# Kernel tuning notes

Measured on AMD Instinct MI355X. Metric: run time of the kernel, lower is better.

Reference implementation:

```python
import jax, jax.numpy as jnp
import numpy as np
import math

N_BLOCKS, DEPTH, K = 5, 10, 2


def build_dilations():
    # Mirrors WaveNet.__init__: list of (new_dilation, init_dilation) per layer.
    dil = []
    init = 1
    for _ in range(N_BLOCKS):
        new = 1
        for _ in range(DEPTH):
            dil.append((new, init))
            init = new
            new *= 2
    return dil


def conv1d_k2(x, w):
    # x: [N, Cin, L], w: [Cout, Cin, 2]; VALID conv -> [N, Cout, L-1]
    return jax.lax.conv_general_dilated(x, w, (1,), 'VALID',
                                        dimension_numbers=('NCH', 'OIH', 'NCH'))


def pw(x, w):
    # 1x1 conv: x [N, Cin, L], w [Cout, Cin]
    return jnp.einsum('oi,nil->nol', w, x)


def dilate(x, dilation, init_dilation):
    # Faithful port of the pytorch-wavenet dilate(): refolds time into batch.
    # All shape arithmetic is static Python ints (jit-safe).
    r = dilation / init_dilation
    if r == 1:
        return x
    n, c, l = x.shape
    new_l = int(math.ceil(l / r) * r)
    if new_l != l:
        x = jnp.pad(x, ((0, 0), (0, 0), (new_l - l, 0)))  # pad_start with zeros
        l = new_l
    l_new = int(round(l * init_dilation / dilation))
    n_new = int(round(n * dilation / init_dilation))
    x = jnp.transpose(x, (1, 2, 0)).reshape(c, l_new, n_new)  # (c, l, n) row-major view
    return jnp.transpose(x, (2, 0, 1))


def wavenet_forward(tokens, emb, pre_w, filt_w, gate_w, res_w, skip_w,
                    post_w1, post_b1, post_w2, post_b2):
    # preprocess: embedding -> [B, C_res, L], then causal k=2 conv (length preserved)
    x = jnp.transpose(emb[tokens], (0, 2, 1))
    x = conv1d_k2(jnp.pad(x, ((0, 0), (0, 0), (K - 1, 0))), pre_w)
    skip = None
    for i, (d, init_d) in enumerate(build_dilations()):
        xd = dilate(x, d, init_d)                       # fold/unfold to dilation d
        z = jnp.tanh(conv1d_k2(xd, filt_w[i])) * jax.nn.sigmoid(conv1d_k2(xd, gate_w[i]))
        s = pw(dilate(z, 1, d), skip_w[i])              # skip contribution, unfolded
        x = pw(z, res_w[i]) + xd[:, :, K - 1:]          # residual connection (folded)
        skip = s if skip is None else skip[:, :, -s.shape[2]:] + s
    h = jax.nn.relu(skip)
    h = jax.nn.relu(pw(h, post_w1) + post_b1[None, :, None])
    return pw(h, post_w2) + post_b2[None, :, None]


def setup_inputs() -> dict:
    key = jax.random.key(0)
    ks = jax.random.split(key, 11)
    B, L = 4, 8192
    V, Cr, Cd, Cs, Ce = 256, 32, 32, 512, 256
    NL = N_BLOCKS * DEPTH
    f = lambda k, shape: jax.random.normal(k, shape, jnp.float32) * 0.1
    return {
        'tokens': jax.random.randint(ks[0], (B, L), 0, V, dtype=jnp.int32),
        'emb': f(ks[1], (V, Cr)),
        'pre_w': f(ks[2], (Cr, Cr, K)),
        'filt_w': f(ks[3], (NL, Cd, Cr, K)),
        'gate_w': f(ks[4], (NL, Cd, Cr, K)),
        'res_w': f(ks[5], (NL, Cr, Cd)),
        'skip_w': f(ks[6], (NL, Cs, Cd)),
        'post_w1': f(ks[7], (Ce, Cs)),
        'post_b1': f(ks[8], (Ce,)),
        'post_w2': f(ks[9], (V, Ce)),
        'post_b2': f(ks[10], (V,)),
    }


def reference(tokens, emb, pre_w, filt_w, gate_w, res_w, skip_w,
              post_w1, post_b1, post_w2, post_b2):
    return wavenet_forward(tokens, emb, pre_w, filt_w, gate_w, res_w, skip_w,
                           post_w1, post_b1, post_w2, post_b2)
```

## Files before the change

### kernel.cpp

```cpp
#include <hip/hip_runtime.h>
#include <math.h>

#define NB 4
#define L0 8192
#define CR 32
#define CD 32
#define CS 512
#define CE 256
#define NV 256
#define OUT_T 5632
#define XSTRIDE 8192
#define NL 50
#define KCAT 1600

typedef __attribute__((ext_vector_type(8))) short  short8;
typedef __attribute__((ext_vector_type(4))) float  f32x4;
typedef __attribute__((ext_vector_type(4))) float  f4;
typedef __attribute__((ext_vector_type(4))) unsigned short us4;

static __device__ __forceinline__ unsigned short f2bf(float f) {
    unsigned int u = __builtin_bit_cast(unsigned int, f);
    u = (u + 0x7FFFu + ((u >> 16) & 1u)) >> 16;
    return (unsigned short)u;
}

__global__ __launch_bounds__(256) void k_prep(const float* __restrict__ sw,
                                              const float* __restrict__ w1,
                                              const float* __restrict__ w2,
                                              unsigned short* __restrict__ wsb,
                                              unsigned short* __restrict__ w1b,
                                              unsigned short* __restrict__ w2b)
{
    int idx = blockIdx.x * 256 + threadIdx.x;
    if (idx < NL * CS * CD) {
        int l = idx >> 14;
        int co = (idx >> 5) & 511;
        int c = idx & 31;
        wsb[co * KCAT + l * 32 + c] = f2bf(sw[idx]);
    } else if (idx < NL * CS * CD + CE * CS) {
        int e = idx - NL * CS * CD;
        w1b[e] = f2bf(w1[e]);
    } else {
        int e = idx - NL * CS * CD - CE * CS;
        w2b[e] = f2bf(w2[e]);
    }
}

__global__ __launch_bounds__(256) void k_pre(const int* __restrict__ tokens,
                                             const float* __restrict__ emb,
                                             const float* __restrict__ pw,
                                             float* __restrict__ x)
{
    int idx = blockIdx.x * 256 + threadIdx.x;
    int t = idx & (L0 - 1);
    int o = (idx >> 13) & 31;
    int b = idx >> 18;
    const int* tb = tokens + b * L0;
    int tok = tb[t];
    const float* e1 = emb + tok * CR;
    const float* w = pw + o * CR * 2;
    float acc = 0.f;
    if (t > 0) {
        const float* e0 = emb + tb[t - 1] * CR;
#pragma unroll
        for (int i = 0; i < CR; ++i)
            acc += w[i * 2] * e0[i] + w[i * 2 + 1] * e1[i];
    } else {
#pragma unroll
        for (int i = 0; i < CR; ++i)
            acc += w[i * 2 + 1] * e1[i];
    }
    x[(b * CR + o) * XSTRIDE + t] = acc;
}

__global__ __launch_bounds__(256) void k_layer(
    const float* __restrict__ x_in, float* __restrict__ x_out,
    unsigned short* __restrict__ Zt,
    const float* __restrict__ fw, const float* __restrict__ gw,
    const float* __restrict__ rw,
    int T_out, int d, int P, int skipOff, int kOff)
{
    __shared__ float As[32][68];
    __shared__ float Bs[32][68];
    __shared__ float Zs[32][68];
    __shared__ unsigned short ZsT[64][32];
    __shared__ float wfT[64][33];
    __shared__ float wgT[64][33];
    __shared__ float rwT[32][33];
    const int tid = threadIdx.x;
    const int t0 = blockIdx.x * 64;
    const int b = blockIdx.y;
    const float* xb = x_in + b * CR * XSTRIDE;

    for (int e = tid; e < 2048; e += 256) {
        int c = e >> 6, i2 = e & 63;
        wfT[i2][c] = fw[e];
        wgT[i2][c] = gw[e];
    }
    for (int e = tid; e < 1024; e += 256) {
        int c = e >> 5, i = e & 31;
        rwT[i][c] = rw[e];
    }
    {
        int ch = tid >> 3;
        int j0 = (tid & 7) * 8;
        const float* row = xb + ch * XSTRIDE;
#pragma unroll
        for (int k = 0; k < 8; ++k) {
            int t = t0 + j0 + k;
            float a = 0.f, bb = 0.f;
            if (t < T_out) {
                if (t >= P) a = row[t - P];
                bb = row[t + d - P];
            }
            As[ch][j0 + k] = a;
            Bs[ch][j0 + k] = bb;
        }
    }
    __syncthreads();
    {
        int c = tid & 31;
        int j0 = (tid >> 5) * 8;
        float af[8] = {0, 0, 0, 0, 0, 0, 0, 0};
        float ag[8] = {0, 0, 0, 0, 0, 0, 0, 0};
#pragma unroll
        for (int i = 0; i < 32; ++i) {
            float av[8], bv[8];
            *(f4*)&av[0] = *(const f4*)&As[i][j0];
            *(f4*)&av[4] = *(const f4*)&As[i][j0 + 4];
            *(f4*)&bv[0] = *(const f4*)&Bs[i][j0];
            *(f4*)&bv[4] = *(const f4*)&Bs[i][j0 + 4];
            float f0 = wfT[2 * i][c], f1 = wfT[2 * i + 1][c];
            float g0 = wgT[2 * i][c], g1 = wgT[2 * i + 1][c];
#pragma unroll
            for (int k = 0; k < 8; ++k) {
                af[k] += f0 * av[k] + f1 * bv[k];
                ag[k] += g0 * av[k] + g1 * bv[k];
            }
        }
#pragma unroll
        for (int k = 0; k < 8; ++k) {
            float e2a = __expf(2.f * af[k]);
            float th = 1.f - __fdividef(2.f, e2a + 1.f);
            float sg = __fdividef(1.f, 1.f + __expf(-ag[k]));
            float z = th * sg;
            Zs[c][j0 + k] = z;
            ZsT[j0 + k][c] = f2bf(z);
        }
    }
    __syncthreads();
    {
        int ch = tid >> 3;
        int j0 = (tid & 7) * 8;
        float accv[8];
        *(f4*)&accv[0] = *(const f4*)&Bs[ch][j0];
        *(f4*)&accv[4] = *(const f4*)&Bs[ch][j0 + 4];
#pragma unroll
        for (int i = 0; i < 32; ++i) {
            float w = rwT[i][ch];
            float zv[8];
            *(f4*)&zv[0] = *(const f4*)&Zs[i][j0];
            *(f4*)&zv[4] = *(const f4*)&Zs[i][j0 + 4];
#pragma unroll
            for (int k = 0; k < 8; ++k)
                accv[k] += w * zv[k];
        }
        float* orow = x_out + (b * CR + ch) * XSTRIDE;
#pragma unroll
        for (int k = 0; k < 8; ++k) {
            int t = t0 + j0 + k;
            if (t < T_out) orow[t] = accv[k];
        }
    }
    {
        int tl = tid >> 2;
        int cq = (tid & 3) * 8;
        int t = t0 + tl;
        if (t >= skipOff && t < T_out) {
            unsigned short* dst =
                Zt + ((size_t)b * OUT_T + (t - skipOff)) * KCAT + kOff + cq;
            *(short8*)dst = *(const short8*)&ZsT[tl][cq];
        }
    }
}

template <int MODE>
__global__ __launch_bounds__(256) void k_gemm(
    const unsigned short* __restrict__ A,
    const unsigned short* __restrict__ B,
    const float* __restrict__ bias,
    void* __restrict__ Cout, int M, int K)
{
    __shared__ unsigned short Asm[128][72];
    __shared__ unsigned short Bsm[64][72];
    const int tid = threadIdx.x;
    const int n0 = blockIdx.x * 64;
    const int m0 = blockIdx.y * 128;
    const int b = blockIdx.z;
    const unsigned short* Bb = B + (size_t)b * OUT_T * K;
    const int lane = tid & 63;
    const int wm = tid >> 6;
    f32x4 acc[2][4];
#pragma unroll
    for (int fm = 0; fm < 2; ++fm)
#pragma unroll
        for (int fn = 0; fn < 4; ++fn)
            acc[fm][fn] = (f32x4){0.f, 0.f, 0.f, 0.f};

    for (int kb = 0; kb < K; kb += 64) {
        __syncthreads();
#pragma unroll
        for (int it = 0; it < 4; ++it) {
            int lin = tid + it * 256;
            int row = lin >> 3, c8 = (lin & 7) * 8;
            *(short8*)&Asm[row][c8] =
                *(const short8*)&A[(size_t)(m0 + row) * K + kb + c8];
        }
#pragma unroll
        for (int it = 0; it < 2; ++it) {
            int lin = tid + it * 256;
            int row = lin >> 3, c8 = (lin & 7) * 8;
            *(short8*)&Bsm[row][c8] =
                *(const short8*)&Bb[(size_t)(n0 + row) * K + kb + c8];
        }
        __syncthreads();
#pragma unroll
        for (int kk = 0; kk < 2; ++kk) {
            short8 a[2], bb[4];
#pragma unroll
            for (int fm = 0; fm < 2; ++fm)
                a[fm] = *(const short8*)&Asm[wm * 32 + fm * 16 + (lane & 15)]
                                           [kk * 32 + (lane >> 4) * 8];
#pragma unroll
            for (int fn = 0; fn < 4; ++fn)
                bb[fn] = *(const short8*)&Bsm[fn * 16 + (lane & 15)]
                                            [kk * 32 + (lane >> 4) * 8];
#pragma unroll
            for (int fm = 0; fm < 2; ++fm)
#pragma unroll
                for (int fn = 0; fn < 4; ++fn)
                    acc[fm][fn] = __builtin_amdgcn_mfma_f32_16x16x32_bf16(
                        a[fm], bb[fn], acc[fm][fn], 0, 0, 0);
        }
    }
#pragma unroll
    for (int fm = 0; fm < 2; ++fm) {
        int mb = m0 + wm * 32 + fm * 16 + (lane >> 4) * 4;
#pragma unroll
        for (int fn = 0; fn < 4; ++fn) {
            int n = n0 + fn * 16 + (lane & 15);
            float v[4];
#pragma unroll
            for (int r = 0; r < 4; ++r) {
                v[r] = acc[fm][fn][r];
                if (MODE >= 1) v[r] += bias[mb + r];
                if (MODE <= 1) v[r] = v[r] > 0.f ? v[r] : 0.f;
            }
            if (MODE == 2) {
                float* o = (float*)Cout;
#pragma unroll
                for (int r = 0; r < 4; ++r)
                    o[((size_t)b * NV + mb + r) * OUT_T + n] = v[r];
            } else {
                unsigned short* o = (unsigned short*)Cout;
                us4 pk;
#pragma unroll
                for (int r = 0; r < 4; ++r) pk[r] = f2bf(v[r]);
                *(us4*)&o[((size_t)b * OUT_T + n) * M + mb] = pk;
            }
        }
    }
}

extern "C" void kernel_launch(void* const* d_in, const int* in_sizes, int n_in,
                              void* d_out, int out_size, void* d_ws, size_t ws_size,
                              hipStream_t stream)
{
    const int*   tokens  = (const int*)d_in[0];
    const float* emb     = (const float*)d_in[1];
    const float* pre_w   = (const float*)d_in[2];
    const float* filt_w  = (const float*)d_in[3];
    const float* gate_w  = (const float*)d_in[4];
    const float* res_w   = (const float*)d_in[5];
    const float* skip_w  = (const float*)d_in[6];
    const float* post_w1 = (const float*)d_in[7];
    const float* post_b1 = (const float*)d_in[8];
    const float* post_w2 = (const float*)d_in[9];
    const float* post_b2 = (const float*)d_in[10];
    float* out = (float*)d_out;

    char* ws = (char*)d_ws;
    float* xA = (float*)ws;                 ws += (size_t)NB * CR * XSTRIDE * 4;
    float* xB = (float*)ws;                 ws += (size_t)NB * CR * XSTRIDE * 4;
    unsigned short* Zt    = (unsigned short*)ws; ws += (size_t)NB * OUT_T * KCAT * 2;
    unsigned short* skipT = (unsigned short*)ws; ws += (size_t)NB * OUT_T * CS * 2;
    unsigned short* h1T   = (unsigned short*)ws; ws += (size_t)NB * OUT_T * CE * 2;
    unsigned short* wsb   = (unsigned short*)ws; ws += (size_t)CS * KCAT * 2;
    unsigned short* w1b   = (unsigned short*)ws; ws += (size_t)CE * CS * 2;
    unsigned short* w2b   = (unsigned short*)ws; ws += (size_t)NV * CE * 2;

    k_prep<<<3968, 256, 0, stream>>>(skip_w, post_w1, post_w2, wsb, w1b, w2b);
    k_pre<<<(NB * CR * L0) / 256, 256, 0, stream>>>(tokens, emb, pre_w, xA);

    int T = L0;
    int init = 1;
    float* xin = xA;
    float* xout = xB;
    int li = 0;
    for (int blk = 0; blk < 5; ++blk) {
        int nw = 1;
        for (int j = 0; j < 10; ++j) {
            int d = nw;
            int P = 0;
            if (d > init) {
                int r = d / init;
                int l = T / init;
                int nl = ((l + r - 1) / r) * r;
                P = (nl - l) * init;
            }
            int T_out = T + P - d;
            dim3 grid((T_out + 63) / 64, NB);
            k_layer<<<grid, 256, 0, stream>>>(
                xin, xout, Zt,
                filt_w + (size_t)li * CD * CR * 2,
                gate_w + (size_t)li * CD * CR * 2,
                res_w + (size_t)li * CR * CD,
                T_out, d, P, T_out - OUT_T, li * 32);
            float* tmp = xin; xin = xout; xout = tmp;
            T = T_out;
            init = d;
            nw <<= 1;
            ++li;
        }
    }

    dim3 gs(OUT_T / 64, CS / 128, NB);
    k_gemm<0><<<gs, 256, 0, stream>>>(wsb, Zt, nullptr, skipT, CS, KCAT);
    dim3 g1(OUT_T / 64, CE / 128, NB);
    k_gemm<1><<<g1, 256, 0, stream>>>(w1b, skipT, post_b1, h1T, CE, CS);
    dim3 g2(OUT_T / 64, NV / 128, NB);
    k_gemm<2><<<g2, 256, 0, stream>>>(w2b, h1T, post_b2, out, NV, CE);
}
```

Baseline: 1.451 ms.

## Fuse preprocess and all residual layers into one cooperative persistent kernel

Replaces the preprocess launch and the 50 per-layer launches with a single cooperative kernel of 512 blocks. The per-layer schedule (T_out, dilation, padding) is precomputed on the host and passed as a struct, and the layers are separated by grid-wide syncs. The aim is to remove per-launch overhead and inter-kernel gaps between the many small layer kernels. In exchange it pays a grid.sync per layer, and blocks sit idle once later layers need fewer tiles. If the cooperative launch fails, it falls back to the old per-layer launches.

```diff
diff --git a/kernel.cpp b/kernel.cpp
--- a/kernel.cpp
+++ b/kernel.cpp
@@ -1,4 +1,5 @@
 #include <hip/hip_runtime.h>
+#include <hip/hip_cooperative_groups.h>
 #include <math.h>
 
 #define NB 4
@@ -17,6 +18,8 @@
 typedef __attribute__((ext_vector_type(4))) float  f32x4;
 typedef __attribute__((ext_vector_type(4))) float  f4;
 typedef __attribute__((ext_vector_type(4))) unsigned short us4;
+
+struct Sched { int T_out[NL]; int d[NL]; int P[NL]; };
 
 static __device__ __forceinline__ unsigned short f2bf(float f) {
     unsigned int u = __builtin_bit_cast(unsigned int, f);
@@ -56,8 +59,7 @@
     int o = (idx >> 13) & 31;
     int b = idx >> 18;
     const int* tb = tokens + b * L0;
-    int tok = tb[t];
-    const float* e1 = emb + tok * CR;
+    const float* e1 = emb + tb[t] * CR;
     const float* w = pw + o * CR * 2;
     float acc = 0.f;
     if (t > 0) {
@@ -73,33 +75,33 @@
     x[(b * CR + o) * XSTRIDE + t] = acc;
 }
 
-__global__ __launch_bounds__(256) void k_layer(
+struct LayerSmem {
+    float As[32][68];
+    float Bs[32][68];
+    float Zs[32][68];
+    unsigned short ZsT[64][32];
+    float wfT[64][33];
+    float wgT[64][33];
+    float rwT[32][33];
+};
+
+static __device__ __forceinline__ void layer_tile(
+    LayerSmem& sm, int tid, int b, int t0,
     const float* __restrict__ x_in, float* __restrict__ x_out,
     unsigned short* __restrict__ Zt,
     const float* __restrict__ fw, const float* __restrict__ gw,
     const float* __restrict__ rw,
     int T_out, int d, int P, int skipOff, int kOff)
 {
-    __shared__ float As[32][68];
-    __shared__ float Bs[32][68];
-    __shared__ float Zs[32][68];
-    __shared__ unsigned short ZsT[64][32];
-    __shared__ float wfT[64][33];
-    __shared__ float wgT[64][33];
-    __shared__ float rwT[32][33];
-    const int tid = threadIdx.x;
-    const int t0 = blockIdx.x * 64;
-    const int b = blockIdx.y;
     const float* xb = x_in + b * CR * XSTRIDE;
-
     for (int e = tid; e < 2048; e += 256) {
         int c = e >> 6, i2 = e & 63;
-        wfT[i2][c] = fw[e];
-        wgT[i2][c] = gw[e];
+        sm.wfT[i2][c] = fw[e];
+        sm.wgT[i2][c] = gw[e];
     }
     for (int e = tid; e < 1024; e += 256) {
         int c = e >> 5, i = e & 31;
-        rwT[i][c] = rw[e];
+        sm.rwT[i][c] = rw[e];
     }
     {
         int ch = tid >> 3;
@@ -113,8 +115,8 @@
                 if (t >= P) a = row[t - P];
                 bb = row[t + d - P];
             }
-            As[ch][j0 + k] = a;
-            Bs[ch][j0 + k] = bb;
+            sm.As[ch][j0 + k] = a;
+            sm.Bs[ch][j0 + k] = bb;
         }
     }
     __syncthreads();
@@ -126,12 +128,12 @@
 #pragma unroll
         for (int i = 0; i < 32; ++i) {
             float av[8], bv[8];
-            *(f4*)&av[0] = *(const f4*)&As[i][j0];
-            *(f4*)&av[4] = *(const f4*)&As[i][j0 + 4];
-            *(f4*)&bv[0] = *(const f4*)&Bs[i][j0];
-            *(f4*)&bv[4] = *(const f4*)&Bs[i][j0 + 4];
-            float f0 = wfT[2 * i][c], f1 = wfT[2 * i + 1][c];
-            float g0 = wgT[2 * i][c], g1 = wgT[2 * i + 1][c];
+            *(f4*)&av[0] = *(const f4*)&sm.As[i][j0];
+            *(f4*)&av[4] = *(const f4*)&sm.As[i][j0 + 4];
+            *(f4*)&bv[0] = *(const f4*)&sm.Bs[i][j0];
+            *(f4*)&bv[4] = *(const f4*)&sm.Bs[i][j0 + 4];
+            float f0 = sm.wfT[2 * i][c], f1 = sm.wfT[2 * i + 1][c];
+            float g0 = sm.wgT[2 * i][c], g1 = sm.wgT[2 * i + 1][c];
 #pragma unroll
             for (int k = 0; k < 8; ++k) {
                 af[k] += f0 * av[k] + f1 * bv[k];
@@ -144,8 +146,8 @@
             float th = 1.f - __fdividef(2.f, e2a + 1.f);
             float sg = __fdividef(1.f, 1.f + __expf(-ag[k]));
             float z = th * sg;
-            Zs[c][j0 + k] = z;
-            ZsT[j0 + k][c] = f2bf(z);
+            sm.Zs[c][j0 + k] = z;
+            sm.ZsT[j0 + k][c] = f2bf(z);
         }
     }
     __syncthreads();
@@ -153,14 +155,14 @@
         int ch = tid >> 3;
         int j0 = (tid & 7) * 8;
         float accv[8];
-        *(f4*)&accv[0] = *(const f4*)&Bs[ch][j0];
-        *(f4*)&accv[4] = *(const f4*)&Bs[ch][j0 + 4];
+        *(f4*)&accv[0] = *(const f4*)&sm.Bs[ch][j0];
+        *(f4*)&accv[4] = *(const f4*)&sm.Bs[ch][j0 + 4];
 #pragma unroll
         for (int i = 0; i < 32; ++i) {
-            float w = rwT[i][ch];
+            float w = sm.rwT[i][ch];
             float zv[8];
-            *(f4*)&zv[0] = *(const f4*)&Zs[i][j0];
-            *(f4*)&zv[4] = *(const f4*)&Zs[i][j0 + 4];
+            *(f4*)&zv[0] = *(const f4*)&sm.Zs[i][j0];
+            *(f4*)&zv[4] = *(const f4*)&sm.Zs[i][j0 + 4];
 #pragma unroll
             for (int k = 0; k < 8; ++k)
                 accv[k] += w * zv[k];
@@ -179,9 +181,73 @@
         if (t >= skipOff && t < T_out) {
             unsigned short* dst =
                 Zt + ((size_t)b * OUT_T + (t - skipOff)) * KCAT + kOff + cq;
-            *(short8*)dst = *(const short8*)&ZsT[tl][cq];
-        }
-    }
+            *(short8*)dst = *(const short8*)&sm.ZsT[tl][cq];
+        }
+    }
+}
+
+__global__ __launch_bounds__(256, 2) void k_fused(
+    const int* __restrict__ tokens, const float* __restrict__ emb,
+    const float* __restrict__ pre_w,
+    const float* __restrict__ filt_w, const float* __restrict__ gate_w,
+    const float* __restrict__ res_w,
+    float* __restrict__ xA, float* __restrict__ xB,
+    unsigned short* __restrict__ Zt, Sched s)
+{
+    cooperative_groups::grid_group grid = cooperative_groups::this_grid();
+    const int tid = threadIdx.x;
+    __shared__ LayerSmem sm;
+
+    for (int idx = blockIdx.x * 256 + tid; idx < NB * CR * L0; idx += gridDim.x * 256) {
+        int t = idx & (L0 - 1);
+        int o = (idx >> 13) & 31;
+        int b = idx >> 18;
+        const int* tb = tokens + b * L0;
+        const float* e1 = emb + tb[t] * CR;
+        const float* w = pre_w + o * CR * 2;
+        float acc = 0.f;
+        if (t > 0) {
+            const float* e0 = emb + tb[t - 1] * CR;
+#pragma unroll
+            for (int i = 0; i < CR; ++i)
+                acc += w[i * 2] * e0[i] + w[i * 2 + 1] * e1[i];
+        } else {
+#pragma unroll
+            for (int i = 0; i < CR; ++i)
+                acc += w[i * 2 + 1] * e1[i];
+        }
+        xA[(b * CR + o) * XSTRIDE + t] = acc;
+    }
+    grid.sync();
+
+    for (int li = 0; li < NL; ++li) {
+        const float* x_in = (li & 1) ? xB : xA;
+        float* x_out = (li & 1) ? xA : xB;
+        const int T_out = s.T_out[li];
+        const int ntiles = (T_out + 63) >> 6;
+        if ((int)blockIdx.x < ntiles * NB) {
+            const int b = blockIdx.x / ntiles;
+            const int t0 = (blockIdx.x - b * ntiles) * 64;
+            layer_tile(sm, tid, b, t0, x_in, x_out, Zt,
+                       filt_w + (size_t)li * CD * CR * 2,
+                       gate_w + (size_t)li * CD * CR * 2,
+                       res_w + (size_t)li * CR * CD,
+                       T_out, s.d[li], s.P[li], T_out - OUT_T, li * 32);
+        }
+        grid.sync();
+    }
+}
+
+__global__ __launch_bounds__(256) void k_layer(
+    const float* __restrict__ x_in, float* __restrict__ x_out,
+    unsigned short* __restrict__ Zt,
+    const float* __restrict__ fw, const float* __restrict__ gw,
+    const float* __restrict__ rw,
+    int T_out, int d, int P, int skipOff, int kOff)
+{
+    __shared__ LayerSmem sm;
+    layer_tile(sm, threadIdx.x, blockIdx.y, blockIdx.x * 64,
+               x_in, x_out, Zt, fw, gw, rw, T_out, d, P, skipOff, kOff);
 }
 
 template <int MODE>
@@ -300,37 +366,46 @@
     unsigned short* w2b   = (unsigned short*)ws; ws += (size_t)NV * CE * 2;
 
     k_prep<<<3968, 256, 0, stream>>>(skip_w, post_w1, post_w2, wsb, w1b, w2b);
-    k_pre<<<(NB * CR * L0) / 256, 256, 0, stream>>>(tokens, emb, pre_w, xA);
-
-    int T = L0;
-    int init = 1;
-    float* xin = xA;
-    float* xout = xB;
-    int li = 0;
-    for (int blk = 0; blk < 5; ++blk) {
-        int nw = 1;
-        for (int j = 0; j < 10; ++j) {
-            int d = nw;
-            int P = 0;
-            if (d > init) {
-                int r = d / init;
-                int l = T / init;
-                int nl = ((l + r - 1) / r) * r;
-                P = (nl - l) * init;
+
+    Sched s;
+    {
+        int T = L0, init = 1, li = 0;
+        for (int blk = 0; blk < 5; ++blk) {
+            int nw = 1;
+            for (int j = 0; j < 10; ++j) {
+                int d = nw, P = 0;
+                if (d > init) {
+                    int r = d / init;
+                    int l = T / init;
+                    int nl = ((l + r - 1) / r) * r;
+                    P = (nl - l) * init;
+                }
+                int T_out = T + P - d;
+                s.T_out[li] = T_out; s.d[li] = d; s.P[li] = P;
+                T = T_out; init = d; nw <<= 1; ++li;
             }
-            int T_out = T + P - d;
+        }
+    }
+
+    const int* tk = tokens;
+    void* args[] = {(void*)&tk, (void*)&emb, (void*)&pre_w,
+                    (void*)&filt_w, (void*)&gate_w, (void*)&res_w,
+                    (void*)&xA, (void*)&xB, (void*)&Zt, (void*)&s};
+    hipError_t cerr = hipLaunchCooperativeKernel((const void*)k_fused, dim3(512),
+                                                 dim3(256), args, 0, stream);
+    if (cerr != hipSuccess) {
+        k_pre<<<(NB * CR * L0) / 256, 256, 0, stream>>>(tokens, emb, pre_w, xA);
+        float* xin = xA; float* xout = xB;
+        for (int li = 0; li < NL; ++li) {
+            int T_out = s.T_out[li];
             dim3 grid((T_out + 63) / 64, NB);
             k_layer<<<grid, 256, 0, stream>>>(
                 xin, xout, Zt,
                 filt_w + (size_t)li * CD * CR * 2,
                 gate_w + (size_t)li * CD * CR * 2,
                 res_w + (size_t)li * CR * CD,
-                T_out, d, P, T_out - OUT_T, li * 32);
+                T_out, s.d[li], s.P[li], T_out - OUT_T, li * 32);
             float* tmp = xin; xin = xout; xout = tmp;
-            T = T_out;
-            init = d;
-            nw <<= 1;
-            ++li;
         }
     }
 
```

Result: slower. 5.195 ms (+258.0%).

## Fuse consecutive WaveNet layer pairs into one kernel with LDS-resident intermediates

Applied to the files above, without the earlier changes.

Replaces the per-layer kernel with a kernel that processes two consecutive dilated layers per launch, loading four shifted input tiles and keeping the intermediate residual output in shared memory. This halves the layer launches and removes the global round-trip of the intermediate activation between paired layers. In exchange it recomputes the first layer's gate for two offset tiles, uses a large dynamic LDS footprint (about 140KB) and 512-thread blocks that limit occupancy to one block per CU. It also uses 128-wide time tiles, which gives fewer blocks per launch.

```diff
diff --git a/kernel.cpp b/kernel.cpp
--- a/kernel.cpp
+++ b/kernel.cpp
@@ -12,6 +12,7 @@
 #define XSTRIDE 8192
 #define NL 50
 #define KCAT 1600
+#define TW 128
 
 typedef __attribute__((ext_vector_type(8))) short  short8;
 typedef __attribute__((ext_vector_type(4))) float  f32x4;
@@ -56,8 +57,7 @@
     int o = (idx >> 13) & 31;
     int b = idx >> 18;
     const int* tb = tokens + b * L0;
-    int tok = tb[t];
-    const float* e1 = emb + tok * CR;
+    const float* e1 = emb + tb[t] * CR;
     const float* w = pw + o * CR * 2;
     float acc = 0.f;
     if (t > 0) {
@@ -73,113 +73,193 @@
     x[(b * CR + o) * XSTRIDE + t] = acc;
 }
 
-__global__ __launch_bounds__(256) void k_layer(
-    const float* __restrict__ x_in, float* __restrict__ x_out,
+struct PairSmem {
+    float T00[32][136];
+    float T01[32][136];
+    float T10[32][136];
+    float T11[32][136];
+    float ZA[32][136];
+    float ZB[32][136];
+    float wfT[64][33];
+    float wgT[64][33];
+    float rwT[32][33];
+    unsigned short ZsT[2][128][32];
+};
+static_assert(sizeof(PairSmem) <= 160 * 1024, "LDS overflow");
+
+static __device__ __forceinline__ void gate_tile(
+    const float (*__restrict__ X0)[136], const float (*__restrict__ X1)[136],
+    float (*__restrict__ Zf)[136], unsigned short (*__restrict__ Zb)[32],
+    const float (*__restrict__ wf)[33], const float (*__restrict__ wg)[33],
+    int c, int j0)
+{
+    float af[8] = {0, 0, 0, 0, 0, 0, 0, 0};
+    float ag[8] = {0, 0, 0, 0, 0, 0, 0, 0};
+#pragma unroll
+    for (int i = 0; i < 32; ++i) {
+        float av[8], bv[8];
+        *(f4*)&av[0] = *(const f4*)&X0[i][j0];
+        *(f4*)&av[4] = *(const f4*)&X0[i][j0 + 4];
+        *(f4*)&bv[0] = *(const f4*)&X1[i][j0];
+        *(f4*)&bv[4] = *(const f4*)&X1[i][j0 + 4];
+        float f0 = wf[2 * i][c], f1 = wf[2 * i + 1][c];
+        float g0 = wg[2 * i][c], g1 = wg[2 * i + 1][c];
+#pragma unroll
+        for (int k = 0; k < 8; ++k) {
+            af[k] += f0 * av[k] + f1 * bv[k];
+            ag[k] += g0 * av[k] + g1 * bv[k];
+        }
+    }
+#pragma unroll
+    for (int k = 0; k < 8; ++k) {
+        float e2a = __expf(2.f * af[k]);
+        float th = 1.f - __fdividef(2.f, e2a + 1.f);
+        float sg = __fdividef(1.f, 1.f + __expf(-ag[k]));
+        float z = th * sg;
+        Zf[c][j0 + k] = z;
+        Zb[j0 + k][c] = f2bf(z);
+    }
+}
+
+static __device__ __forceinline__ void resid_tile(
+    const float (*__restrict__ Xd)[136], const float (*__restrict__ Zf)[136],
+    const float (*__restrict__ rw)[33], float* __restrict__ out, int ch, int j0)
+{
+    *(f4*)&out[0] = *(const f4*)&Xd[ch][j0];
+    *(f4*)&out[4] = *(const f4*)&Xd[ch][j0 + 4];
+#pragma unroll
+    for (int i = 0; i < 32; ++i) {
+        float w = rw[i][ch];
+        float zv[8];
+        *(f4*)&zv[0] = *(const f4*)&Zf[i][j0];
+        *(f4*)&zv[4] = *(const f4*)&Zf[i][j0 + 4];
+#pragma unroll
+        for (int k = 0; k < 8; ++k)
+            out[k] += w * zv[k];
+    }
+}
+
+__global__ __launch_bounds__(512, 1) void k_pair(
+    const float* __restrict__ x0, float* __restrict__ x_out,
     unsigned short* __restrict__ Zt,
-    const float* __restrict__ fw, const float* __restrict__ gw,
-    const float* __restrict__ rw,
-    int T_out, int d, int P, int skipOff, int kOff)
-{
-    __shared__ float As[32][68];
-    __shared__ float Bs[32][68];
-    __shared__ float Zs[32][68];
-    __shared__ unsigned short ZsT[64][32];
-    __shared__ float wfT[64][33];
-    __shared__ float wgT[64][33];
-    __shared__ float rwT[32][33];
+    const float* __restrict__ fw1, const float* __restrict__ gw1,
+    const float* __restrict__ rw1,
+    const float* __restrict__ fw2, const float* __restrict__ gw2,
+    const float* __restrict__ rw2,
+    int T0, int T1, int T2, int d1, int d2, int P1, int P2,
+    int skip1, int skip2, int kOff1, int kOff2)
+{
+    extern __shared__ char smraw[];
+    PairSmem& sm = *reinterpret_cast<PairSmem*>(smraw);
     const int tid = threadIdx.x;
-    const int t0 = blockIdx.x * 64;
     const int b = blockIdx.y;
-    const float* xb = x_in + b * CR * XSTRIDE;
-
-    for (int e = tid; e < 2048; e += 256) {
+    const int t0 = blockIdx.x * TW;
+    const int baseA = t0 - P2;
+    const int baseB = t0 + d2 - P2;
+
+    for (int e = tid; e < 2048; e += 512) {
         int c = e >> 6, i2 = e & 63;
-        wfT[i2][c] = fw[e];
-        wgT[i2][c] = gw[e];
-    }
-    for (int e = tid; e < 1024; e += 256) {
-        int c = e >> 5, i = e & 31;
-        rwT[i][c] = rw[e];
-    }
-    {
-        int ch = tid >> 3;
-        int j0 = (tid & 7) * 8;
-        const float* row = xb + ch * XSTRIDE;
+        sm.wfT[i2][c] = fw1[e];
+        sm.wgT[i2][c] = gw1[e];
+    }
+    for (int e = tid; e < 1024; e += 512)
+        sm.rwT[e & 31][e >> 5] = rw1[e];
+    {
+        int ch = tid >> 4;
+        int j0 = (tid & 15) * 8;
+        const float* row = x0 + ((size_t)b * CR + ch) * XSTRIDE;
+        const int bases[4] = {baseA, baseA + d1, baseB, baseB + d1};
+        float* const dsts[4] = {&sm.T00[ch][j0], &sm.T01[ch][j0],
+                                &sm.T10[ch][j0], &sm.T11[ch][j0]};
+#pragma unroll
+        for (int q = 0; q < 4; ++q) {
+            int iu0 = bases[q] + j0 - P1;
+            float v[8];
+            if (iu0 >= 0 && iu0 + 7 < T0) {
+#pragma unroll
+                for (int k = 0; k < 8; ++k) v[k] = row[iu0 + k];
+            } else {
+#pragma unroll
+                for (int k = 0; k < 8; ++k) {
+                    int iu = iu0 + k;
+                    v[k] = (iu >= 0 && iu < T0) ? row[iu] : 0.f;
+                }
+            }
+#pragma unroll
+            for (int k = 0; k < 8; ++k) dsts[q][k] = v[k];
+        }
+    }
+    __syncthreads();
+
+    {
+        int c = tid & 31;
+        int j0 = (tid >> 5) * 8;
+        gate_tile(sm.T00, sm.T01, sm.ZA, sm.ZsT[0], sm.wfT, sm.wgT, c, j0);
+        gate_tile(sm.T10, sm.T11, sm.ZB, sm.ZsT[1], sm.wfT, sm.wgT, c, j0);
+    }
+    __syncthreads();
+
+    for (int e = tid; e < 2048; e += 512) {
+        int c = e >> 6, i2 = e & 63;
+        sm.wfT[i2][c] = fw2[e];
+        sm.wgT[i2][c] = gw2[e];
+    }
+#pragma unroll
+    for (int s = 0; s < 2; ++s) {
+        int lin = tid + s * 512;
+        int tile = lin >> 9;
+        int r = lin & 511;
+        int j = r >> 2, cq = (r & 3) * 8;
+        int u = (tile ? baseB : baseA) + j;
+        if (u >= skip1 && u < T1) {
+            unsigned short* dst =
+                Zt + ((size_t)b * OUT_T + (u - skip1)) * KCAT + kOff1 + cq;
+            *(short8*)dst = *(const short8*)&sm.ZsT[tile][j][cq];
+        }
+    }
+    {
+        int ch = tid >> 4;
+        int j0 = (tid & 15) * 8;
+        float acc[8];
+        resid_tile(sm.T01, sm.ZA, sm.rwT, acc, ch, j0);
+#pragma unroll
+        for (int k = 0; k < 8; ++k)
+            sm.T00[ch][j0 + k] = (t0 + j0 + k >= P2) ? acc[k] : 0.f;
+        resid_tile(sm.T11, sm.ZB, sm.rwT, acc, ch, j0);
+#pragma unroll
+        for (int k = 0; k < 8; ++k)
+            sm.T10[ch][j0 + k] = acc[k];
+    }
+    __syncthreads();
+
+    for (int e = tid; e < 1024; e += 512)
+        sm.rwT[e & 31][e >> 5] = rw2[e];
+    {
+        int c = tid & 31;
+        int j0 = (tid >> 5) * 8;
+        gate_tile(sm.T00, sm.T10, sm.ZA, sm.ZsT[0], sm.wfT, sm.wgT, c, j0);
+    }
+    __syncthreads();
+
+    {
+        int j = tid >> 2, cq = (tid & 3) * 8;
+        int t = t0 + j;
+        if (t >= skip2 && t < T2) {
+            unsigned short* dst =
+                Zt + ((size_t)b * OUT_T + (t - skip2)) * KCAT + kOff2 + cq;
+            *(short8*)dst = *(const short8*)&sm.ZsT[0][j][cq];
+        }
+    }
+    {
+        int ch = tid >> 4;
+        int j0 = (tid & 15) * 8;
+        float acc[8];
+        resid_tile(sm.T10, sm.ZA, sm.rwT, acc, ch, j0);
+        float* orow = x_out + ((size_t)b * CR + ch) * XSTRIDE;
 #pragma unroll
         for (int k = 0; k < 8; ++k) {
             int t = t0 + j0 + k;
-            float a = 0.f, bb = 0.f;
-            if (t < T_out) {
-                if (t >= P) a = row[t - P];
-                bb = row[t + d - P];
-            }
-            As[ch][j0 + k] = a;
-            Bs[ch][j0 + k] = bb;
-        }
-    }
-    __syncthreads();
-    {
-        int c = tid & 31;
-        int j0 = (tid >> 5) * 8;
-        float af[8] = {0, 0, 0, 0, 0, 0, 0, 0};
-        float ag[8] = {0, 0, 0, 0, 0, 0, 0, 0};
-#pragma unroll
-        for (int i = 0; i < 32; ++i) {
-            float av[8], bv[8];
-            *(f4*)&av[0] = *(const f4*)&As[i][j0];
-            *(f4*)&av[4] = *(const f4*)&As[i][j0 + 4];
-            *(f4*)&bv[0] = *(const f4*)&Bs[i][j0];
-            *(f4*)&bv[4] = *(const f4*)&Bs[i][j0 + 4];
-            float f0 = wfT[2 * i][c], f1 = wfT[2 * i + 1][c];
-            float g0 = wgT[2 * i][c], g1 = wgT[2 * i + 1][c];
-#pragma unroll
-            for (int k = 0; k < 8; ++k) {
-                af[k] += f0 * av[k] + f1 * bv[k];
-                ag[k] += g0 * av[k] + g1 * bv[k];
-            }
-        }
-#pragma unroll
-        for (int k = 0; k < 8; ++k) {
-            float e2a = __expf(2.f * af[k]);
-            float th = 1.f - __fdividef(2.f, e2a + 1.f);
-            float sg = __fdividef(1.f, 1.f + __expf(-ag[k]));
-            float z = th * sg;
-            Zs[c][j0 + k] = z;
-            ZsT[j0 + k][c] = f2bf(z);
-        }
-    }
-    __syncthreads();
-    {
-        int ch = tid >> 3;
-        int j0 = (tid & 7) * 8;
-        float accv[8];
-        *(f4*)&accv[0] = *(const f4*)&Bs[ch][j0];
-        *(f4*)&accv[4] = *(const f4*)&Bs[ch][j0 + 4];
-#pragma unroll
-        for (int i = 0; i < 32; ++i) {
-            float w = rwT[i][ch];
-            float zv[8];
-            *(f4*)&zv[0] = *(const f4*)&Zs[i][j0];
-            *(f4*)&zv[4] = *(const f4*)&Zs[i][j0 + 4];
-#pragma unroll
-            for (int k = 0; k < 8; ++k)
-                accv[k] += w * zv[k];
-        }
-        float* orow = x_out + (b * CR + ch) * XSTRIDE;
-#pragma unroll
-        for (int k = 0; k < 8; ++k) {
-            int t = t0 + j0 + k;
-            if (t < T_out) orow[t] = accv[k];
-        }
-    }
-    {
-        int tl = tid >> 2;
-        int cq = (tid & 3) * 8;
-        int t = t0 + tl;
-        if (t >= skipOff && t < T_out) {
-            unsigned short* dst =
-                Zt + ((size_t)b * OUT_T + (t - skipOff)) * KCAT + kOff + cq;
-            *(short8*)dst = *(const short8*)&ZsT[tl][cq];
+            if (t < T2) orow[t] = acc[k];
         }
     }
 }
@@ -302,36 +382,45 @@
     k_prep<<<3968, 256, 0, stream>>>(skip_w, post_w1, post_w2, wsb, w1b, w2b);
     k_pre<<<(NB * CR * L0) / 256, 256, 0, stream>>>(tokens, emb, pre_w, xA);
 
-    int T = L0;
-    int init = 1;
+    int dArr[NL], pArr[NL], tArr[NL];
+    {
+        int T = L0, init = 1, li = 0;
+        for (int blk = 0; blk < 5; ++blk) {
+            int nw = 1;
+            for (int j = 0; j < 10; ++j) {
+                int d = nw, P = 0;
+                if (d > init) {
+                    int r = d / init;
+                    int l = T / init;
+                    int nl = ((l + r - 1) / r) * r;
+                    P = (nl - l) * init;
+                }
+                int T_out = T + P - d;
+                dArr[li] = d; pArr[li] = P; tArr[li] = T_out;
+                T = T_out; init = d; nw <<= 1; ++li;
+            }
+        }
+    }
+
     float* xin = xA;
     float* xout = xB;
-    int li = 0;
-    for (int blk = 0; blk < 5; ++blk) {
-        int nw = 1;
-        for (int j = 0; j < 10; ++j) {
-            int d = nw;
-            int P = 0;
-            if (d > init) {
-                int r = d / init;
-                int l = T / init;
-                int nl = ((l + r - 1) / r) * r;
-                P = (nl - l) * init;
-            }
-            int T_out = T + P - d;
-            dim3 grid((T_out + 63) / 64, NB);
-            k_layer<<<grid, 256, 0, stream>>>(
-                xin, xout, Zt,
-                filt_w + (size_t)li * CD * CR * 2,
-                gate_w + (size_t)li * CD * CR * 2,
-                res_w + (size_t)li * CR * CD,
-                T_out, d, P, T_out - OUT_T, li * 32);
-            float* tmp = xin; xin = xout; xout = tmp;
-            T = T_out;
-            init = d;
-            nw <<= 1;
-            ++li;
-        }
+    for (int p = 0; p < 25; ++p) {
+        int l1 = 2 * p, l2 = 2 * p + 1;
+        int T0 = (l1 == 0) ? L0 : tArr[l1 - 1];
+        int T1 = tArr[l1], T2 = tArr[l2];
+        int ntiles = (T2 + TW - 1) / TW;
+        dim3 grid(ntiles, NB);
+        k_pair<<<grid, 512, sizeof(PairSmem), stream>>>(
+            xin, xout, Zt,
+            filt_w + (size_t)l1 * CD * CR * 2,
+            gate_w + (size_t)l1 * CD * CR * 2,
+            res_w + (size_t)l1 * CR * CD,
+            filt_w + (size_t)l2 * CD * CR * 2,
+            gate_w + (size_t)l2 * CD * CR * 2,
+            res_w + (size_t)l2 * CR * CD,
+            T0, T1, T2, dArr[l1], dArr[l2], pArr[l1], pArr[l2],
+            T1 - OUT_T, T2 - OUT_T, l1 * 32, l2 * 32);
+        float* tmp = xin; xin = xout; xout = tmp;
     }
 
     dim3 gs(OUT_T / 64, CS / 128, NB);
```

After: 1.642 ms. +13.2%, slower.
